# Kernel optimization log

Measured on AMD Instinct MI355X. Metric: run time of the kernel, lower is better.

Reference implementation:

```python
import jax, jax.numpy as jnp
import numpy as np

N = 1026     # tickers (hardcoded in original module)
T = 8        # price window length; self.T = T-1 = 7
H = 64       # hidden dim
F_IN = 5     # price features
E = 1026     # number of hyperedges
NNZ = 200000 # incidence entries per hypergraph


def leaky(x):
    return jnp.where(x >= 0, x, 0.2 * x)


def gru_fwd(x, Wih, Whh, bih, bhh):
    # torch.nn.GRU, batch_first. x: [N, T, F_IN] -> full [N,T,H], last [N,H]
    def step(h, xt):
        gi = xt @ Wih.T + bih
        gh = h @ Whh.T + bhh
        ir, iz, inn = jnp.split(gi, 3, axis=-1)
        hr, hz, hn = jnp.split(gh, 3, axis=-1)
        r = jax.nn.sigmoid(ir + hr)
        z = jax.nn.sigmoid(iz + hz)
        n = jnp.tanh(inn + r * hn)
        h = (1.0 - z) * n + z * h
        return h, h
    h0 = jnp.zeros((x.shape[0], H), x.dtype)
    last, full = jax.lax.scan(step, h0, jnp.swapaxes(x, 0, 1))
    return jnp.swapaxes(full, 0, 1), last


def hyp_conv(x, idx, theta, bias):
    # PyG HypergraphConv (use_attention=False): out = D^-1 H B^-1 H^T (X theta) + bias
    node, edge = idx[0], idx[1]
    ones = jnp.ones(node.shape, x.dtype)
    deg_n = jax.ops.segment_sum(ones, node, num_segments=N)
    deg_e = jax.ops.segment_sum(ones, edge, num_segments=E)
    Dinv = jnp.where(deg_n > 0, 1.0 / deg_n, 0.0)
    Binv = jnp.where(deg_e > 0, 1.0 / deg_e, 0.0)
    xt = x @ theta
    e = jax.ops.segment_sum(xt[node] * Binv[edge][:, None], edge, num_segments=E)
    out = jax.ops.segment_sum(e[edge], node, num_segments=N) * Dinv[:, None]
    return out + bias


def decayed_attention(query, context, Win, Wout, ae, ab):
    # query [N,1,H], context [N,T,H]; 'general' attention with temporal-decay term
    q = jnp.einsum('nod,de->noe', query, Win)
    w = jax.nn.softmax(jnp.einsum('nod,ntd->not', q, context), axis=-1)  # [N,1,T]
    mix = w * jnp.swapaxes(context, 1, 2)                                # [N,H,T]
    delta = jnp.arange(T - 1, -1, -1, dtype=context.dtype).reshape(1, 1, T)
    bt = jnp.exp(-ab * delta)                                            # [N,1,T]
    term2 = jax.nn.relu(ae * mix * bt)
    mixs = jnp.sum(term2 + mix, axis=-1)[:, None, :]                     # [N,1,H]
    comb = jnp.concatenate([mixs, q], axis=2).reshape(N, 2 * H)
    return jnp.tanh(comb @ Wout).reshape(N, H), w


def _forward(price_input, hyp_T, hyp, Wih, Whh, bih, bhh, Win, Wout, ae, ab,
             theta1, bias1, theta2, bias2, w1, w2, a_param, Wl, bl):
    context, last = gru_fwd(price_input, Wih, Whh, bih, bhh)
    output, _ = decayed_attention(last[:, None, :], context, Win, Wout, ae, ab)  # [N,H]

    def per_t(idx):
        x1 = leaky(hyp_conv(output, idx, theta1, bias1))
        return leaky(hyp_conv(x1, idx, theta2, bias2))

    x2 = jax.vmap(per_t)(hyp_T)            # [T, N, H]
    sub = x2[1:] - x2[:-1]                 # diff(): [T-1, N, H]
    b = jnp.mean(sub, axis=(1, 2), keepdims=True)
    U = 1.0 / (1.0 + a_param * (b - sub))  # c = 1
    z = ((U * sub) / U).sum(axis=(1, 2))   # [T-1] (faithful to original)
    wattn = jax.nn.softmax(w2 @ leaky(w1 @ z), axis=0)  # [T-1]
    concat = wattn[:, None, None] * sub
    xx1 = concat[0] + concat[2]            # stack([0],[2]) then sum over dim 0
    xg = leaky(hyp_conv(output, hyp, theta1, bias1))
    xg = leaky(hyp_conv(xg, hyp, theta2, bias2))
    oput = jnp.concatenate([xg, xx1], axis=1)  # [N, 2H]
    return leaky(oput @ Wl + bl)               # [N, 1]


def setup_inputs() -> dict:
    key = jax.random.key(0)
    ks = jax.random.split(key, 24)
    def xn(k, shape, scale=None):
        fan = (shape[-2] + shape[-1]) if len(shape) >= 2 else shape[0]
        s = scale if scale is not None else float(np.sqrt(2.0 / fan))
        return jax.random.normal(k, shape, dtype=jnp.float32) * s
    inp = {}
    inp['price_input'] = jax.random.normal(ks[0], (N, T, F_IN), dtype=jnp.float32)
    node_T = jax.random.randint(ks[1], (T, 1, NNZ), 0, N)
    edge_T = jax.random.randint(ks[2], (T, 1, NNZ), 0, E)
    inp['hyp_T'] = jnp.concatenate([node_T, edge_T], axis=1).astype(jnp.int32)
    node = jax.random.randint(ks[3], (1, NNZ), 0, N)
    edge = jax.random.randint(ks[4], (1, NNZ), 0, E)
    inp['hyp'] = jnp.concatenate([node, edge], axis=0).astype(jnp.int32)
    inp['Wih'] = xn(ks[5], (3 * H, F_IN))
    inp['Whh'] = xn(ks[6], (3 * H, H))
    std = float(1.0 / np.sqrt(3 * H))
    inp['bih'] = jax.random.uniform(ks[7], (3 * H,), minval=-std, maxval=std, dtype=jnp.float32)
    inp['bhh'] = jax.random.uniform(ks[8], (3 * H,), minval=-std, maxval=std, dtype=jnp.float32)
    inp['Win'] = xn(ks[9], (H, H))
    inp['Wout'] = xn(ks[10], (2 * H, H))
    inp['ae'] = xn(ks[11], (N, 1, 1), scale=0.05)
    inp['ab'] = jnp.abs(xn(ks[12], (N, 1, 1), scale=0.05))
    inp['theta1'] = xn(ks[13], (H, H))
    inp['bias1'] = jax.random.uniform(ks[14], (H,), minval=-0.125, maxval=0.125, dtype=jnp.float32)
    inp['theta2'] = xn(ks[15], (H, H))
    inp['bias2'] = jax.random.uniform(ks[16], (H,), minval=-0.125, maxval=0.125, dtype=jnp.float32)
    inp['w1'] = xn(ks[17], (H, T - 1))
    inp['w2'] = xn(ks[18], (T - 1, H))
    inp['a_param'] = xn(ks[19], (T - 1, 1, 1), scale=0.05)
    inp['Wl'] = xn(ks[20], (2 * H, 1))
    inp['bl'] = jax.random.uniform(ks[21], (1,), minval=-0.088, maxval=0.088, dtype=jnp.float32)
    return inp


def reference(price_input, hyp_T, hyp, Wih, Whh, bih, bhh, Win, Wout, ae, ab,
              theta1, bias1, theta2, bias2, w1, w2, a_param, Wl, bl):
    return _forward(price_input, hyp_T, hyp, Wih, Whh, bih, bhh, Win, Wout, ae, ab,
                    theta1, bias1, theta2, bias2, w1, w2, a_param, Wl, bl)
```

## Files before the change

### kernel.cpp

```cpp
#include <hip/hip_runtime.h>
#include <hip/hip_bf16.h>
#include <math.h>

#define N 1026
#define T 8
#define H 64
#define F_IN 5
#define E 1026
#define NNZ 200000
#define TM 7
#define NG 9
#define KP 1056
#define NWB 132
#define RT 96
#define NT 11
#define NH (N*H)
#define BZC 32
#define CHUNK (NH/BZC)

#define OFF_PRICE   0
#define OFF_WIH     41040
#define OFF_WHH     42000
#define OFF_BIH     54288
#define OFF_BHH     54480
#define OFF_WIN     54672
#define OFF_WOUT    58768
#define OFF_AE      66960
#define OFF_AB      67986
#define OFF_TH1     69012
#define OFF_B1      73108
#define OFF_TH2     73172
#define OFF_B2      77268
#define OFF_W1      77332
#define OFF_W2      77780
#define OFF_APAR    78228
#define OFF_WL      78235
#define OFF_BL      78363
#define TOT_CVT     78364

typedef unsigned int u32;
typedef unsigned short u16;
typedef short bf16x8 __attribute__((ext_vector_type(8)));
typedef float f32x4 __attribute__((ext_vector_type(4)));

__device__ __forceinline__ float leakyf(float x){ return x >= 0.f ? x : 0.2f*x; }
__device__ __forceinline__ float bfbits2f(u16 u){
  union { u32 i; float f; } c; c.i = ((u32)u) << 16; return c.f;
}
__device__ __forceinline__ u16 f2bf(float f){
  u32 x = __builtin_bit_cast(u32, f);
  u32 r = x + 0x7FFFu + ((x >> 16) & 1u);
  return (u16)(r >> 16);
}
__device__ __forceinline__ int detect_f32(const u16* __restrict__ w){
  int lane = threadIdx.x & 63;
  int big = 0;
  for (int k = lane; k < 960; k += 64){
    float a = fabsf(bfbits2f(w[k]));
    if (!(a < 1e3f)) big = 1;
  }
  return (__ballot(big != 0) != 0ull) ? 1 : 0;
}

struct CvtPtrs { const void* p[18]; };

__global__ __launch_bounds__(256) void k_cvt(CvtPtrs ps, float* __restrict__ dst){
  const int offs[19] = {OFF_PRICE, OFF_WIH, OFF_WHH, OFF_BIH, OFF_BHH, OFF_WIN,
                        OFF_WOUT, OFF_AE, OFF_AB, OFF_TH1, OFF_B1, OFF_TH2,
                        OFF_B2, OFF_W1, OFF_W2, OFF_APAR, OFF_WL, OFF_BL, TOT_CVT};
  int isf32 = detect_f32((const u16*)ps.p[1]);
  int i = blockIdx.x*256 + threadIdx.x;
  if (i < TOT_CVT){
    int t = 0;
    #pragma unroll
    for (int k = 1; k < 18; k++) if (i >= offs[k]) t = k;
    int j = i - offs[t];
    float v;
    if (isf32) v = ((const float*)ps.p[t])[j];
    else       v = bfbits2f(((const u16*)ps.p[t])[j]);
    dst[i] = v;
  }
}

__global__ __launch_bounds__(1024) void k_build(const int* __restrict__ hypT,
                                                const int* __restrict__ hyp,
                                                u16* __restrict__ AHm,
                                                u16* __restrict__ AHmT,
                                                float* __restrict__ Dinv,
                                                float* __restrict__ Binv){
  __shared__ u32 bins[RT*NWB];
  int tid = threadIdx.x;
  int g = blockIdx.y, side = blockIdx.z;
  int r0 = blockIdx.x * RT;
  for (int k = tid; k < RT*NWB; k += 1024) bins[k] = 0;
  __syncthreads();
  const int4* np4; const int4* ep4;
  if (g < 8){ const int* np_ = hypT + (size_t)g*2*NNZ;
              np4 = (const int4*)np_; ep4 = (const int4*)(np_ + NNZ); }
  else      { np4 = (const int4*)hyp; ep4 = (const int4*)(hyp + NNZ); }
  #pragma unroll 4
  for (int i = tid; i < NNZ/4; i += 1024){
    int4 a4 = np4[i], b4 = ep4[i];
    int ra[4], ca[4];
    if (side){
      ra[0]=b4.x; ra[1]=b4.y; ra[2]=b4.z; ra[3]=b4.w;
      ca[0]=a4.x; ca[1]=a4.y; ca[2]=a4.z; ca[3]=a4.w;
    } else {
      ra[0]=a4.x; ra[1]=a4.y; ra[2]=a4.z; ra[3]=a4.w;
      ca[0]=b4.x; ca[1]=b4.y; ca[2]=b4.z; ca[3]=b4.w;
    }
    #pragma unroll
    for (int e = 0; e < 4; e++){
      int rr = ra[e] - r0;
      if ((unsigned)rr < (unsigned)RT)
        atomicAdd(&bins[rr*NWB + (ca[e]>>3)], 1u << ((ca[e]&7)*4));
    }
  }
  __syncthreads();
  {
    int r = tid >> 3, j = tid & 7;
    if (r < RT){
      u32 s = 0;
      for (int w = j; w < NWB; w += 8){
        u32 v = bins[r*NWB + w];
        u32 a = (v & 0x0F0F0F0Fu) + ((v >> 4) & 0x0F0F0F0Fu);
        s += (a * 0x01010101u) >> 24;
      }
      s += __shfl_xor(s, 1); s += __shfl_xor(s, 2); s += __shfl_xor(s, 4);
      int gr = r0 + r;
      if (j == 0 && gr < N){
        float inv = s ? 1.f/(float)s : 0.f;
        (side ? Binv : Dinv)[g*N + gr] = inv;
      }
    }
  }
  u16* dst = (side ? AHmT : AHm) + (size_t)g*KP*KP;
  for (int idx = tid; idx < RT*NWB; idx += 1024){
    int rr = idx / NWB, w = idx - rr*NWB;
    u32 v = bins[rr*NWB + w];
    bf16x8 o;
    #pragma unroll
    for (int j = 0; j < 8; j++)
      o[j] = (short)f2bf((float)((v >> (4*j)) & 0xFu));
    *(bf16x8*)(dst + (size_t)(r0 + rr)*KP + w*8) = o;
  }
}

__global__ __launch_bounds__(256) void k_gruattn(const float* __restrict__ price,
                                                 const float* __restrict__ Wih,
                                                 const float* __restrict__ Whh,
                                                 const float* __restrict__ bih,
                                                 const float* __restrict__ bhh,
                                                 const float* __restrict__ Win,
                                                 const float* __restrict__ Wout,
                                                 const float* __restrict__ ae,
                                                 const float* __restrict__ ab,
                                                 float* __restrict__ outp){
  __shared__ float gi[T][192];
  __shared__ float sh[64];
  __shared__ float sctx[T*64];
  __shared__ float part[4][192];
  __shared__ float sx[T*F_IN];
  __shared__ float sq[64];
  __shared__ float ssc[T];
  __shared__ float sco[128];
  int tid = threadIdx.x, w = tid>>6, lane = tid&63;
  int n = blockIdx.x;
  float wr_[16], wz_[16], wn_[16];
  #pragma unroll
  for (int j = 0; j < 16; j++){
    int d = w*16 + j;
    wr_[j] = Whh[(size_t)(      lane)*64 + d];
    wz_[j] = Whh[(size_t)( 64 + lane)*64 + d];
    wn_[j] = Whh[(size_t)(128 + lane)*64 + d];
  }
  if (tid < T*F_IN) sx[tid] = price[(size_t)n*T*F_IN + tid];
  if (tid < 64) sh[tid] = 0.f;
  __syncthreads();
  for (int idx = tid; idx < T*192; idx += 256){
    int t = idx / 192, gd = idx - t*192;
    float acc = bih[gd];
    #pragma unroll
    for (int d5 = 0; d5 < F_IN; d5++)
      acc = fmaf(sx[t*F_IN + d5], Wih[gd*F_IN + d5], acc);
    gi[t][gd] = acc;
  }
  __syncthreads();
  for (int t = 0; t < T; t++){
    float pr = 0.f, pz = 0.f, pn = 0.f;
    #pragma unroll
    for (int j = 0; j < 16; j++){
      float hv = sh[w*16 + j];
      pr = fmaf(hv, wr_[j], pr);
      pz = fmaf(hv, wz_[j], pz);
      pn = fmaf(hv, wn_[j], pn);
    }
    part[w][lane] = pr; part[w][64 + lane] = pz; part[w][128 + lane] = pn;
    __syncthreads();
    if (tid < 64){
      int o = tid;
      float hr = bhh[o]       + part[0][o]     + part[1][o]     + part[2][o]     + part[3][o];
      float hz = bhh[64 + o]  + part[0][64+o]  + part[1][64+o]  + part[2][64+o]  + part[3][64+o];
      float hn = bhh[128 + o] + part[0][128+o] + part[1][128+o] + part[2][128+o] + part[3][128+o];
      float r  = 1.f/(1.f + expf(-(gi[t][o] + hr)));
      float z  = 1.f/(1.f + expf(-(gi[t][64 + o] + hz)));
      float nn = tanhf(gi[t][128 + o] + r*hn);
      float hnew = (1.f - z)*nn + z*sh[o];
      sh[o] = hnew;
      sctx[t*64 + o] = hnew;
    }
    __syncthreads();
  }
  {
    float qp = 0.f;
    #pragma unroll
    for (int j = 0; j < 16; j++)
      qp = fmaf(sh[w*16 + j], Win[(size_t)(w*16 + j)*64 + lane], qp);
    part[w][lane] = qp;
  }
  __syncthreads();
  if (tid < 64) sq[tid] = part[0][tid] + part[1][tid] + part[2][tid] + part[3][tid];
  __syncthreads();
  if (tid < T){
    float s = 0.f;
    for (int d = 0; d < 64; d++) s = fmaf(sq[d], sctx[tid*64 + d], s);
    ssc[tid] = s;
  }
  __syncthreads();
  if (tid < 64){
    int o = tid;
    float m = ssc[0];
    for (int t = 1; t < T; t++) m = fmaxf(m, ssc[t]);
    float wv[T]; float den = 0.f;
    for (int t = 0; t < T; t++){ wv[t] = expf(ssc[t] - m); den += wv[t]; }
    float aen = ae[n], abn = ab[n];
    float mixs = 0.f;
    for (int t = 0; t < T; t++){
      float wt = wv[t]/den;
      float mx = wt * sctx[t*64 + o];
      float bt = expf(-abn * (float)(T-1-t));
      mixs += fmaxf(aen*mx*bt, 0.f) + mx;
    }
    sco[o] = mixs; sco[64 + o] = sq[o];
  }
  __syncthreads();
  {
    float op = 0.f;
    #pragma unroll
    for (int j = 0; j < 32; j++)
      op = fmaf(sco[w*32 + j], Wout[(size_t)(w*32 + j)*64 + lane], op);
    part[w][lane] = op;
  }
  __syncthreads();
  if (tid < 64){
    float o = part[0][tid] + part[1][tid] + part[2][tid] + part[3][tid];
    outp[(size_t)n*H + tid] = tanhf(o);
  }
}

__global__ __launch_bounds__(256) void k_xthetaT(const float* __restrict__ x,
                                                 const float* __restrict__ theta,
                                                 int x_per_graph,
                                                 u16* __restrict__ xtT){
  __shared__ float sth[4096];
  __shared__ float sxr[64][64];
  __shared__ float syt[64][65];
  int tid = threadIdx.x, w = tid>>6, lane = tid&63;
  int g = blockIdx.y;
  int r0 = blockIdx.x*64;
  const float* xg = x + (x_per_graph ? (size_t)g*N*64 : (size_t)0);
  for (int k = tid; k < 1024; k += 256) ((float4*)sth)[k] = ((const float4*)theta)[k];
  for (int rr = w; rr < 64; rr += 4){
    int r = r0 + rr;
    sxr[rr][lane] = (r < N) ? xg[(size_t)r*64 + lane] : 0.f;
  }
  __syncthreads();
  for (int rr = w*16; rr < w*16+16; rr++){
    float acc = 0.f;
    for (int d = 0; d < 64; d++) acc = fmaf(sxr[rr][d], sth[d*64 + lane], acc);
    syt[lane][rr] = acc;
  }
  __syncthreads();
  int col = r0 + lane;
  if (col < KP){
    for (int f = w*16; f < w*16+16; f++)
      xtT[((size_t)g*64 + f)*KP + col] = f2bf(syt[f][lane]);
  }
}

__global__ __launch_bounds__(64) void k_gemm(const u16* __restrict__ A,
                                             const u16* __restrict__ Xt,
                                             int x_per_graph,
                                             const float* __restrict__ scale,
                                             const float* __restrict__ bias,
                                             int mode,
                                             u16* __restrict__ Yt,
                                             float* __restrict__ Yf){
  int g = blockIdx.y;
  int m0 = (blockIdx.x >> 2) * 16;
  int nt = blockIdx.x & 3;
  int lane = threadIdx.x;
  int mrow = lane & 15, quad = lane >> 4;
  const u16* Ap = A + (size_t)g*KP*KP + (size_t)(m0 + mrow)*KP + quad*8;
  const u16* Bp = Xt + (x_per_graph ? (size_t)g*64*KP : (size_t)0)
                     + (size_t)(nt*16 + mrow)*KP + quad*8;
  f32x4 acc = (f32x4){0.f,0.f,0.f,0.f};
  bf16x8 a0 = *(const bf16x8*)Ap;
  bf16x8 b0 = *(const bf16x8*)Bp;
  for (int c = 0; c < 33; c++){
    bf16x8 a1 = a0, b1 = b0;
    if (c < 32){
      a1 = *(const bf16x8*)(Ap + (c+1)*32);
      b1 = *(const bf16x8*)(Bp + (c+1)*32);
    }
    acc = __builtin_amdgcn_mfma_f32_16x16x32_bf16(a0, b0, acc, 0, 0, 0);
    a0 = a1; b0 = b1;
  }
  int mbase = m0 + quad*4;
  float sc_[4];
  #pragma unroll
  for (int r = 0; r < 4; r++){
    int m = mbase + r;
    sc_[r] = (m < N) ? scale[g*N + m] : 0.f;
  }
  if (mode == 0){
    ushort4 o;
    o.x = f2bf(acc[0]*sc_[0]);
    o.y = f2bf(acc[1]*sc_[1]);
    o.z = f2bf(acc[2]*sc_[2]);
    o.w = f2bf(acc[3]*sc_[3]);
    *(ushort4*)(Yt + ((size_t)g*64 + nt*16 + mrow)*KP + mbase) = o;
  } else {
    float bs = bias[nt*16 + mrow];
    #pragma unroll
    for (int r = 0; r < 4; r++){
      int m = mbase + r;
      if (m < N){
        float v = acc[r]*sc_[r] + bs;
        Yf[((size_t)g*N + m)*64 + nt*16 + mrow] = leakyf(v);
      }
    }
  }
}

__global__ __launch_bounds__(256) void k_bz1(const float* __restrict__ x2,
                                             float* __restrict__ bpart){
  int k = blockIdx.x, ch = blockIdx.y, tid = threadIdx.x;
  int wv = tid >> 6, lane = tid & 63;
  const float4* a4 = (const float4*)(x2 + (size_t)k*NH + (size_t)ch*CHUNK);
  const float4* c4 = (const float4*)(x2 + (size_t)(k+1)*NH + (size_t)ch*CHUNK);
  float s = 0.f;
  for (int i = tid; i < CHUNK/4; i += 256){
    float4 cc = c4[i], aa = a4[i];
    s += (cc.x-aa.x)+(cc.y-aa.y)+(cc.z-aa.z)+(cc.w-aa.w);
  }
  __shared__ float red[4];
  for (int off = 32; off; off >>= 1) s += __shfl_down(s, off);
  if (lane == 0) red[wv] = s;
  __syncthreads();
  if (tid == 0) bpart[k*BZC + ch] = red[0]+red[1]+red[2]+red[3];
}

__global__ __launch_bounds__(256) void k_bz2(const float* __restrict__ x2,
                                             const float* __restrict__ bpart,
                                             const float* __restrict__ a_param,
                                             float* __restrict__ zpart){
  int k = blockIdx.x, ch = blockIdx.y, tid = threadIdx.x;
  int wv = tid >> 6, lane = tid & 63;
  __shared__ float sbk;
  if (tid == 0){
    float t = 0.f;
    for (int j = 0; j < BZC; j++) t += bpart[k*BZC + j];
    sbk = t / (float)NH;
  }
  __syncthreads();
  float bk = sbk, ap = a_param[k];
  const float4* a4 = (const float4*)(x2 + (size_t)k*NH + (size_t)ch*CHUNK);
  const float4* c4 = (const float4*)(x2 + (size_t)(k+1)*NH + (size_t)ch*CHUNK);
  float s = 0.f;
  for (int i = tid; i < CHUNK/4; i += 256){
    float4 cc = c4[i], aa = a4[i];
    float sb[4] = {cc.x-aa.x, cc.y-aa.y, cc.z-aa.z, cc.w-aa.w};
    #pragma unroll
    for (int j = 0; j < 4; j++){
      float U = 1.f/(1.f + ap*(bk - sb[j]));
      s += (U*sb[j])/U;
    }
  }
  __shared__ float red[4];
  for (int off = 32; off; off >>= 1) s += __shfl_down(s, off);
  if (lane == 0) red[wv] = s;
  __syncthreads();
  if (tid == 0) zpart[k*BZC + ch] = red[0]+red[1]+red[2]+red[3];
}

__global__ __launch_bounds__(256) void k_final(const float* __restrict__ x2,
                                               const float* __restrict__ zpart,
                                               const float* __restrict__ w1,
                                               const float* __restrict__ w2,
                                               const float* __restrict__ Wl,
                                               const float* __restrict__ bl,
                                               const u16* __restrict__ wihRaw,
                                               void* __restrict__ outv){
  __shared__ float sz[8];
  __shared__ float sy[64];
  __shared__ float swa[8];
  int tid = threadIdx.x;
  int isf32 = detect_f32(wihRaw);
  if (tid < TM){
    float t = 0.f;
    for (int j = 0; j < BZC; j++) t += zpart[tid*BZC + j];
    sz[tid] = t;
  }
  __syncthreads();
  if (tid < 64){
    float y = 0.f;
    for (int kk = 0; kk < TM; kk++) y += w1[tid*TM + kk]*sz[kk];
    sy[tid] = leakyf(y);
  }
  __syncthreads();
  if (tid < TM){
    float v = 0.f;
    for (int d = 0; d < 64; d++) v += w2[tid*64 + d]*sy[d];
    swa[tid] = v;
  }
  __syncthreads();
  if (tid == 0){
    float m = swa[0];
    for (int t = 1; t < TM; t++) m = fmaxf(m, swa[t]);
    float den = 0.f;
    for (int t = 0; t < TM; t++){ swa[t] = expf(swa[t]-m); den += swa[t]; }
    for (int t = 0; t < TM; t++) swa[t] /= den;
  }
  __syncthreads();
  int n = blockIdx.x*256 + tid;
  if (n < N){
    float w0 = swa[0], w2v = swa[2];
    float acc = bl[0];
    for (int h = 0; h < 64; h++){
      float xg = x2[(size_t)8*NH + (size_t)n*64 + h];
      float s0 = x2[(size_t)1*NH + (size_t)n*64 + h] - x2[(size_t)0*NH + (size_t)n*64 + h];
      float s2 = x2[(size_t)3*NH + (size_t)n*64 + h] - x2[(size_t)2*NH + (size_t)n*64 + h];
      float xx = w0*s0 + w2v*s2;
      acc += xg*Wl[h] + xx*Wl[64 + h];
    }
    float r = leakyf(acc);
    if (isf32) ((float*)outv)[n] = r;
    else       ((__hip_bfloat16*)outv)[n] = __float2bfloat16(r);
  }
}

extern "C" void kernel_launch(void* const* d_in, const int* in_sizes, int n_in,
                              void* d_out, int out_size, void* d_ws, size_t ws_size,
                              hipStream_t stream) {
  const int* hypT = (const int*)d_in[1];
  const int* hyp  = (const int*)d_in[2];

  char* p = (char*)d_ws;
  auto alloc = [&](size_t bytes) -> char* {
    char* r = p; p += (bytes + 63) & ~(size_t)63; return r;
  };
  float* cv   = (float*)alloc((size_t)TOT_CVT*4);
  u16* AHm    = (u16*)  alloc((size_t)NG*KP*KP*2);
  u16* AHmT   = (u16*)  alloc((size_t)NG*KP*KP*2);
  float* Dinv = (float*)alloc((size_t)NG*N*4);
  float* Binv = (float*)alloc((size_t)NG*N*4);
  float* outp = (float*)alloc((size_t)N*H*4);
  float* x1   = (float*)alloc((size_t)NG*N*H*4);
  float* x2   = (float*)alloc((size_t)NG*N*H*4);
  float* bpart= (float*)alloc((size_t)TM*BZC*4);
  float* zpart= (float*)alloc((size_t)TM*BZC*4);
  u16* xtT1   = (u16*)  alloc((size_t)64*KP*2);
  u16* xtT2   = (u16*)  alloc((size_t)NG*64*KP*2);
  u16* ebufT  = (u16*)  alloc((size_t)NG*64*KP*2);

  const float* price  = cv + OFF_PRICE;
  const float* Wih    = cv + OFF_WIH;
  const float* Whh    = cv + OFF_WHH;
  const float* bih    = cv + OFF_BIH;
  const float* bhh    = cv + OFF_BHH;
  const float* Win    = cv + OFF_WIN;
  const float* Wout   = cv + OFF_WOUT;
  const float* ae     = cv + OFF_AE;
  const float* ab     = cv + OFF_AB;
  const float* theta1 = cv + OFF_TH1;
  const float* bias1  = cv + OFF_B1;
  const float* theta2 = cv + OFF_TH2;
  const float* bias2  = cv + OFF_B2;
  const float* w1     = cv + OFF_W1;
  const float* w2     = cv + OFF_W2;
  const float* a_par  = cv + OFF_APAR;
  const float* Wl     = cv + OFF_WL;
  const float* bl     = cv + OFF_BL;

  CvtPtrs ps;
  ps.p[0]=d_in[0];  ps.p[1]=d_in[3];  ps.p[2]=d_in[4];  ps.p[3]=d_in[5];
  ps.p[4]=d_in[6];  ps.p[5]=d_in[7];  ps.p[6]=d_in[8];  ps.p[7]=d_in[9];
  ps.p[8]=d_in[10]; ps.p[9]=d_in[11]; ps.p[10]=d_in[12]; ps.p[11]=d_in[13];
  ps.p[12]=d_in[14]; ps.p[13]=d_in[15]; ps.p[14]=d_in[16]; ps.p[15]=d_in[17];
  ps.p[16]=d_in[18]; ps.p[17]=d_in[19];
  k_cvt<<<(TOT_CVT+255)/256, 256, 0, stream>>>(ps, cv);

  k_build<<<dim3(NT, NG, 2), 1024, 0, stream>>>(hypT, hyp, AHm, AHmT, Dinv, Binv);
  k_gruattn<<<N, 256, 0, stream>>>(price, Wih, Whh, bih, bhh,
                                   Win, Wout, ae, ab, outp);

  k_xthetaT<<<dim3(17, 1), 256, 0, stream>>>(outp, theta1, 0, xtT1);
  k_gemm<<<dim3((KP/16)*4, NG), 64, 0, stream>>>(AHmT, xtT1, 0, Binv, nullptr, 0, ebufT, nullptr);
  k_gemm<<<dim3((KP/16)*4, NG), 64, 0, stream>>>(AHm, ebufT, 1, Dinv, bias1, 1, nullptr, x1);

  k_xthetaT<<<dim3(17, NG), 256, 0, stream>>>(x1, theta2, 1, xtT2);
  k_gemm<<<dim3((KP/16)*4, NG), 64, 0, stream>>>(AHmT, xtT2, 1, Binv, nullptr, 0, ebufT, nullptr);
  k_gemm<<<dim3((KP/16)*4, NG), 64, 0, stream>>>(AHm, ebufT, 1, Dinv, bias2, 1, nullptr, x2);

  k_bz1<<<dim3(TM, BZC), 256, 0, stream>>>(x2, bpart);
  k_bz2<<<dim3(TM, BZC), 256, 0, stream>>>(x2, bpart, a_par, zpart);
  k_final<<<(N+255)/256, 256, 0, stream>>>(x2, zpart, w1, w2, Wl, bl,
                                           (const u16*)d_in[3], d_out);
}
```

Before: 271.7 us.

## Split GEMM K-loop across two waves and shrink xtheta tiles for more blocks

The dense incidence GEMM kernel now runs two wavefronts per block. Each wave handles half of the K dimension (17 and 16 chunks), and the partial accumulators are reduced through shared memory before the epilogue. This halves the serial MFMA/load chain per block, which adds latency hiding and parallelism. The x·theta kernel now uses 16-row tiles instead of 64, giving 66 blocks per graph instead of 17, and writes with vectorized ushort4 stores. The cost is an extra barrier and shared-memory reduction per GEMM block, and theta is reloaded by more blocks.

New measurement: 280.3 us. 1.03x slower.

```diff
diff --git a/kernel.cpp b/kernel.cpp
--- a/kernel.cpp
+++ b/kernel.cpp
@@ -263,81 +263,100 @@
                                                  int x_per_graph,
                                                  u16* __restrict__ xtT){
   __shared__ float sth[4096];
-  __shared__ float sxr[64][64];
-  __shared__ float syt[64][65];
+  __shared__ float sxr[16][64];
+  __shared__ float syt[64][17];
   int tid = threadIdx.x, w = tid>>6, lane = tid&63;
   int g = blockIdx.y;
-  int r0 = blockIdx.x*64;
+  int r0 = blockIdx.x*16;
   const float* xg = x + (x_per_graph ? (size_t)g*N*64 : (size_t)0);
   for (int k = tid; k < 1024; k += 256) ((float4*)sth)[k] = ((const float4*)theta)[k];
-  for (int rr = w; rr < 64; rr += 4){
-    int r = r0 + rr;
-    sxr[rr][lane] = (r < N) ? xg[(size_t)r*64 + lane] : 0.f;
-  }
-  __syncthreads();
-  for (int rr = w*16; rr < w*16+16; rr++){
+  {
+    int idx = tid;
+    #pragma unroll
+    for (int i = 0; i < 4; i++, idx += 256){
+      int rr = idx >> 6, d = idx & 63;
+      int r = r0 + rr;
+      sxr[rr][d] = (r < N) ? xg[(size_t)r*64 + d] : 0.f;
+    }
+  }
+  __syncthreads();
+  #pragma unroll
+  for (int rr = 0; rr < 4; rr++){
+    int row = w*4 + rr;
     float acc = 0.f;
-    for (int d = 0; d < 64; d++) acc = fmaf(sxr[rr][d], sth[d*64 + lane], acc);
-    syt[lane][rr] = acc;
-  }
-  __syncthreads();
-  int col = r0 + lane;
-  if (col < KP){
-    for (int f = w*16; f < w*16+16; f++)
-      xtT[((size_t)g*64 + f)*KP + col] = f2bf(syt[f][lane]);
-  }
-}
-
-__global__ __launch_bounds__(64) void k_gemm(const u16* __restrict__ A,
-                                             const u16* __restrict__ Xt,
-                                             int x_per_graph,
-                                             const float* __restrict__ scale,
-                                             const float* __restrict__ bias,
-                                             int mode,
-                                             u16* __restrict__ Yt,
-                                             float* __restrict__ Yf){
+    for (int d = 0; d < 64; d++) acc = fmaf(sxr[row][d], sth[d*64 + lane], acc);
+    syt[lane][row] = acc;
+  }
+  __syncthreads();
+  {
+    int f = tid >> 2, c = (tid & 3)*4;
+    ushort4 o;
+    o.x = f2bf(syt[f][c+0]); o.y = f2bf(syt[f][c+1]);
+    o.z = f2bf(syt[f][c+2]); o.w = f2bf(syt[f][c+3]);
+    *(ushort4*)(xtT + ((size_t)g*64 + f)*KP + r0 + c) = o;
+  }
+}
+
+__global__ __launch_bounds__(128) void k_gemm(const u16* __restrict__ A,
+                                              const u16* __restrict__ Xt,
+                                              int x_per_graph,
+                                              const float* __restrict__ scale,
+                                              const float* __restrict__ bias,
+                                              int mode,
+                                              u16* __restrict__ Yt,
+                                              float* __restrict__ Yf){
+  __shared__ f32x4 part[64];
   int g = blockIdx.y;
   int m0 = (blockIdx.x >> 2) * 16;
   int nt = blockIdx.x & 3;
-  int lane = threadIdx.x;
+  int tid = threadIdx.x;
+  int kh = tid >> 6, lane = tid & 63;
   int mrow = lane & 15, quad = lane >> 4;
-  const u16* Ap = A + (size_t)g*KP*KP + (size_t)(m0 + mrow)*KP + quad*8;
+  int kofs = kh ? 544 : 0;
+  int NC   = kh ? 16  : 17;
+  const u16* Ap = A + (size_t)g*KP*KP + (size_t)(m0 + mrow)*KP + kofs + quad*8;
   const u16* Bp = Xt + (x_per_graph ? (size_t)g*64*KP : (size_t)0)
-                     + (size_t)(nt*16 + mrow)*KP + quad*8;
+                     + (size_t)(nt*16 + mrow)*KP + kofs + quad*8;
   f32x4 acc = (f32x4){0.f,0.f,0.f,0.f};
   bf16x8 a0 = *(const bf16x8*)Ap;
   bf16x8 b0 = *(const bf16x8*)Bp;
-  for (int c = 0; c < 33; c++){
+  for (int c = 0; c < NC; c++){
     bf16x8 a1 = a0, b1 = b0;
-    if (c < 32){
+    if (c + 1 < NC){
       a1 = *(const bf16x8*)(Ap + (c+1)*32);
       b1 = *(const bf16x8*)(Bp + (c+1)*32);
     }
     acc = __builtin_amdgcn_mfma_f32_16x16x32_bf16(a0, b0, acc, 0, 0, 0);
     a0 = a1; b0 = b1;
   }
-  int mbase = m0 + quad*4;
-  float sc_[4];
-  #pragma unroll
-  for (int r = 0; r < 4; r++){
-    int m = mbase + r;
-    sc_[r] = (m < N) ? scale[g*N + m] : 0.f;
-  }
-  if (mode == 0){
-    ushort4 o;
-    o.x = f2bf(acc[0]*sc_[0]);
-    o.y = f2bf(acc[1]*sc_[1]);
-    o.z = f2bf(acc[2]*sc_[2]);
-    o.w = f2bf(acc[3]*sc_[3]);
-    *(ushort4*)(Yt + ((size_t)g*64 + nt*16 + mrow)*KP + mbase) = o;
-  } else {
-    float bs = bias[nt*16 + mrow];
+  if (kh == 1) part[lane] = acc;
+  __syncthreads();
+  if (kh == 0){
+    f32x4 o2 = part[lane];
+    acc[0] += o2[0]; acc[1] += o2[1]; acc[2] += o2[2]; acc[3] += o2[3];
+    int mbase = m0 + quad*4;
+    float sc_[4];
     #pragma unroll
     for (int r = 0; r < 4; r++){
       int m = mbase + r;
-      if (m < N){
-        float v = acc[r]*sc_[r] + bs;
-        Yf[((size_t)g*N + m)*64 + nt*16 + mrow] = leakyf(v);
+      sc_[r] = (m < N) ? scale[g*N + m] : 0.f;
+    }
+    if (mode == 0){
+      ushort4 o;
+      o.x = f2bf(acc[0]*sc_[0]);
+      o.y = f2bf(acc[1]*sc_[1]);
+      o.z = f2bf(acc[2]*sc_[2]);
+      o.w = f2bf(acc[3]*sc_[3]);
+      *(ushort4*)(Yt + ((size_t)g*64 + nt*16 + mrow)*KP + mbase) = o;
+    } else {
+      float bs = bias[nt*16 + mrow];
+      #pragma unroll
+      for (int r = 0; r < 4; r++){
+        int m = mbase + r;
+        if (m < N){
+          float v = acc[r]*sc_[r] + bs;
+          Yf[((size_t)g*N + m)*64 + nt*16 + mrow] = leakyf(v);
+        }
       }
     }
   }
@@ -505,13 +524,13 @@
   k_gruattn<<<N, 256, 0, stream>>>(price, Wih, Whh, bih, bhh,
                                    Win, Wout, ae, ab, outp);
 
-  k_xthetaT<<<dim3(17, 1), 256, 0, stream>>>(outp, theta1, 0, xtT1);
-  k_gemm<<<dim3((KP/16)*4, NG), 64, 0, stream>>>(AHmT, xtT1, 0, Binv, nullptr, 0, ebufT, nullptr);
-  k_gemm<<<dim3((KP/16)*4, NG), 64, 0, stream>>>(AHm, ebufT, 1, Dinv, bias1, 1, nullptr, x1);
-
-  k_xthetaT<<<dim3(17, NG), 256, 0, stream>>>(x1, theta2, 1, xtT2);
-  k_gemm<<<dim3((KP/16)*4, NG), 64, 0, stream>>>(AHmT, xtT2, 1, Binv, nullptr, 0, ebufT, nullptr);
-  k_gemm<<<dim3((KP/16)*4, NG), 64, 0, stream>>>(AHm, ebufT, 1, Dinv, bias2, 1, nullptr, x2);
+  k_xthetaT<<<dim3(KP/16, 1), 256, 0, stream>>>(outp, theta1, 0, xtT1);
+  k_gemm<<<dim3((KP/16)*4, NG), 128, 0, stream>>>(AHmT, xtT1, 0, Binv, nullptr, 0, ebufT, nullptr);
+  k_gemm<<<dim3((KP/16)*4, NG), 128, 0, stream>>>(AHm, ebufT, 1, Dinv, bias1, 1, nullptr, x1);
+
+  k_xthetaT<<<dim3(KP/16, NG), 256, 0, stream>>>(x1, theta2, 1, xtT2);
+  k_gemm<<<dim3((KP/16)*4, NG), 128, 0, stream>>>(AHmT, xtT2, 1, Binv, nullptr, 0, ebufT, nullptr);
+  k_gemm<<<dim3((KP/16)*4, NG), 128, 0, stream>>>(AHm, ebufT, 1, Dinv, bias2, 1, nullptr, x2);
 
   k_bz1<<<dim3(TM, BZC), 256, 0, stream>>>(x2, bpart);
   k_bz2<<<dim3(TM, BZC), 256, 0, stream>>>(x2, bpart, a_par, zpart);
```

## Split incidence-matrix build into partitioned scan and separate expand kernel

Applied to the files above, without the earlier changes.

The single k_build kernel, which scanned all NNZ entries per row tile with 1024 threads, is split into two kernels. k_scan divides the NNZ range into PB=4 parts across more 256-thread blocks and merges its shared-memory nibble bins into a global packed-count array with atomics. k_expand then turns the packed counts into bf16 dense matrices and computes the degree inverses. The aim is more parallelism in the scan phase, at the cost of an extra memset, global atomics, an intermediate buffer and one more launch. If any incidence pair repeats 16 or more times, its 4-bit count can overflow into the neighbouring field during the global atomic merge, as it could in the original shared-memory bins.

New measurement: 314.9 us. 1.16x slower.

```diff
diff --git a/kernel.cpp b/kernel.cpp
--- a/kernel.cpp
+++ b/kernel.cpp
@@ -14,6 +14,7 @@
 #define NWB 132
 #define RT 96
 #define NT 11
+#define PB 4
 #define NH (N*H)
 #define BZC 32
 #define CHUNK (NH/BZC)
@@ -82,24 +83,25 @@
   }
 }
 
-__global__ __launch_bounds__(1024) void k_build(const int* __restrict__ hypT,
-                                                const int* __restrict__ hyp,
-                                                u16* __restrict__ AHm,
-                                                u16* __restrict__ AHmT,
-                                                float* __restrict__ Dinv,
-                                                float* __restrict__ Binv){
+__global__ __launch_bounds__(256) void k_scan(const int* __restrict__ hypT,
+                                              const int* __restrict__ hyp,
+                                              u32* __restrict__ nHm,
+                                              u32* __restrict__ nHmT){
   __shared__ u32 bins[RT*NWB];
   int tid = threadIdx.x;
+  int tile = blockIdx.x / PB, prt = blockIdx.x - tile*PB;
   int g = blockIdx.y, side = blockIdx.z;
-  int r0 = blockIdx.x * RT;
-  for (int k = tid; k < RT*NWB; k += 1024) bins[k] = 0;
+  int r0 = tile * RT;
+  for (int k = tid; k < RT*NWB; k += 256) bins[k] = 0;
   __syncthreads();
   const int4* np4; const int4* ep4;
   if (g < 8){ const int* np_ = hypT + (size_t)g*2*NNZ;
               np4 = (const int4*)np_; ep4 = (const int4*)(np_ + NNZ); }
   else      { np4 = (const int4*)hyp; ep4 = (const int4*)(hyp + NNZ); }
-  #pragma unroll 4
-  for (int i = tid; i < NNZ/4; i += 1024){
+  int i0 = prt * (NNZ/4/PB);
+  int i1 = i0 + (NNZ/4/PB);
+  #pragma unroll 2
+  for (int i = i0 + tid; i < i1; i += 256){
     int4 a4 = np4[i], b4 = ep4[i];
     int ra[4], ca[4];
     if (side){
@@ -117,32 +119,45 @@
     }
   }
   __syncthreads();
-  {
-    int r = tid >> 3, j = tid & 7;
-    if (r < RT){
-      u32 s = 0;
-      for (int w = j; w < NWB; w += 8){
-        u32 v = bins[r*NWB + w];
-        u32 a = (v & 0x0F0F0F0Fu) + ((v >> 4) & 0x0F0F0F0Fu);
-        s += (a * 0x01010101u) >> 24;
-      }
-      s += __shfl_xor(s, 1); s += __shfl_xor(s, 2); s += __shfl_xor(s, 4);
-      int gr = r0 + r;
-      if (j == 0 && gr < N){
-        float inv = s ? 1.f/(float)s : 0.f;
-        (side ? Binv : Dinv)[g*N + gr] = inv;
-      }
-    }
-  }
-  u16* dst = (side ? AHmT : AHm) + (size_t)g*KP*KP;
-  for (int idx = tid; idx < RT*NWB; idx += 1024){
-    int rr = idx / NWB, w = idx - rr*NWB;
-    u32 v = bins[rr*NWB + w];
+  u32* dst = (side ? nHmT : nHm) + (size_t)g*KP*NWB + (size_t)r0*NWB;
+  for (int k = tid; k < RT*NWB; k += 256){
+    u32 v = bins[k];
+    if (v) atomicAdd(dst + k, v);
+  }
+}
+
+__global__ __launch_bounds__(256) void k_expand(const u32* __restrict__ nHm,
+                                                const u32* __restrict__ nHmT,
+                                                u16* __restrict__ AHm,
+                                                u16* __restrict__ AHmT,
+                                                float* __restrict__ Dinv,
+                                                float* __restrict__ Binv){
+  int tid = threadIdx.x;
+  int g = blockIdx.y, side = blockIdx.z;
+  int r0 = blockIdx.x * 16;
+  const u32* src = (side ? nHmT : nHm) + (size_t)g*KP*NWB + (size_t)r0*NWB;
+  u16* dst = (side ? AHmT : AHm) + (size_t)g*KP*KP + (size_t)r0*KP;
+  for (int idx = tid; idx < 16*NWB; idx += 256){
+    u32 v = src[idx];
     bf16x8 o;
     #pragma unroll
     for (int j = 0; j < 8; j++)
       o[j] = (short)f2bf((float)((v >> (4*j)) & 0xFu));
-    *(bf16x8*)(dst + (size_t)(r0 + rr)*KP + w*8) = o;
+    *(bf16x8*)(dst + (size_t)idx*8) = o;
+  }
+  int r = tid >> 4, j = tid & 15;
+  u32 s = 0;
+  for (int w = j; w < NWB; w += 16){
+    u32 v = src[r*NWB + w];
+    u32 a = (v & 0x0F0F0F0Fu) + ((v >> 4) & 0x0F0F0F0Fu);
+    s += (a * 0x01010101u) >> 24;
+  }
+  s += __shfl_xor(s, 1); s += __shfl_xor(s, 2);
+  s += __shfl_xor(s, 4); s += __shfl_xor(s, 8);
+  int gr = r0 + r;
+  if (j == 0 && gr < N){
+    float inv = s ? 1.f/(float)s : 0.f;
+    (side ? Binv : Dinv)[g*N + gr] = inv;
   }
 }
 
@@ -461,6 +476,8 @@
     char* r = p; p += (bytes + 63) & ~(size_t)63; return r;
   };
   float* cv   = (float*)alloc((size_t)TOT_CVT*4);
+  u32* nHm    = (u32*)  alloc((size_t)NG*KP*NWB*4);
+  u32* nHmT   = (u32*)  alloc((size_t)NG*KP*NWB*4);
   u16* AHm    = (u16*)  alloc((size_t)NG*KP*KP*2);
   u16* AHmT   = (u16*)  alloc((size_t)NG*KP*KP*2);
   float* Dinv = (float*)alloc((size_t)NG*N*4);
@@ -493,6 +510,8 @@
   const float* Wl     = cv + OFF_WL;
   const float* bl     = cv + OFF_BL;
 
+  hipMemsetAsync(nHm, 0, (size_t)2*NG*KP*NWB*4, stream);
+
   CvtPtrs ps;
   ps.p[0]=d_in[0];  ps.p[1]=d_in[3];  ps.p[2]=d_in[4];  ps.p[3]=d_in[5];
   ps.p[4]=d_in[6];  ps.p[5]=d_in[7];  ps.p[6]=d_in[8];  ps.p[7]=d_in[9];
@@ -501,7 +520,8 @@
   ps.p[16]=d_in[18]; ps.p[17]=d_in[19];
   k_cvt<<<(TOT_CVT+255)/256, 256, 0, stream>>>(ps, cv);
 
-  k_build<<<dim3(NT, NG, 2), 1024, 0, stream>>>(hypT, hyp, AHm, AHmT, Dinv, Binv);
+  k_scan  <<<dim3(NT*PB, NG, 2), 256, 0, stream>>>(hypT, hyp, nHm, nHmT);
+  k_expand<<<dim3(KP/16, NG, 2), 256, 0, stream>>>(nHm, nHmT, AHm, AHmT, Dinv, Binv);
   k_gruattn<<<N, 256, 0, stream>>>(price, Wih, Whh, bih, bhh,
                                    Win, Wout, ae, ab, outp);
 
```

## Fuse conversion, first theta projection, and temporal sums into neighbouring kernels

Applied to the files above, without the earlier changes.

Moves the dtype-conversion pass into the k_build kernel, with the first column block of each graph converting one slice. The first theta projection and its transposed bf16 store move into the end of the GRU/attention kernel. The two reduction kernels are replaced by per-graph atomic sums in the last GEMM's epilogue, using the algebraic identity that (U*sb)/U equals sb, so each temporal sum becomes S[k+1]-S[k]. This removes four kernel launches and two extra passes over x2. In exchange it relies on float atomics, which give non-deterministic ordering and possible cancellation in the difference of large sums. The padded columns of xtT1 beyond N are also no longer written.

Measured after the change: 280.8 us. 1.03x slower.

```diff
diff --git a/kernel.cpp b/kernel.cpp
--- a/kernel.cpp
+++ b/kernel.cpp
@@ -15,8 +15,6 @@
 #define RT 96
 #define NT 11
 #define NH (N*H)
-#define BZC 32
-#define CHUNK (NH/BZC)
 
 #define OFF_PRICE   0
 #define OFF_WIH     41040
@@ -64,34 +62,37 @@
 
 struct CvtPtrs { const void* p[18]; };
 
-__global__ __launch_bounds__(256) void k_cvt(CvtPtrs ps, float* __restrict__ dst){
-  const int offs[19] = {OFF_PRICE, OFF_WIH, OFF_WHH, OFF_BIH, OFF_BHH, OFF_WIN,
-                        OFF_WOUT, OFF_AE, OFF_AB, OFF_TH1, OFF_B1, OFF_TH2,
-                        OFF_B2, OFF_W1, OFF_W2, OFF_APAR, OFF_WL, OFF_BL, TOT_CVT};
-  int isf32 = detect_f32((const u16*)ps.p[1]);
-  int i = blockIdx.x*256 + threadIdx.x;
-  if (i < TOT_CVT){
-    int t = 0;
-    #pragma unroll
-    for (int k = 1; k < 18; k++) if (i >= offs[k]) t = k;
-    int j = i - offs[t];
-    float v;
-    if (isf32) v = ((const float*)ps.p[t])[j];
-    else       v = bfbits2f(((const u16*)ps.p[t])[j]);
-    dst[i] = v;
-  }
-}
-
 __global__ __launch_bounds__(1024) void k_build(const int* __restrict__ hypT,
                                                 const int* __restrict__ hyp,
                                                 u16* __restrict__ AHm,
                                                 u16* __restrict__ AHmT,
                                                 float* __restrict__ Dinv,
-                                                float* __restrict__ Binv){
+                                                float* __restrict__ Binv,
+                                                CvtPtrs ps,
+                                                float* __restrict__ cv,
+                                                float* __restrict__ Ssum){
   __shared__ u32 bins[RT*NWB];
   int tid = threadIdx.x;
   int g = blockIdx.y, side = blockIdx.z;
   int r0 = blockIdx.x * RT;
+  if (blockIdx.x == 0 && side == 0){
+    const int offs[19] = {OFF_PRICE, OFF_WIH, OFF_WHH, OFF_BIH, OFF_BHH, OFF_WIN,
+                          OFF_WOUT, OFF_AE, OFF_AB, OFF_TH1, OFF_B1, OFF_TH2,
+                          OFF_B2, OFF_W1, OFF_W2, OFF_APAR, OFF_WL, OFF_BL, TOT_CVT};
+    int isf32 = detect_f32((const u16*)ps.p[1]);
+    int i0 = g * 8708;
+    for (int i = i0 + tid; i < i0 + 8708 && i < TOT_CVT; i += 1024){
+      int t = 0;
+      #pragma unroll
+      for (int k = 1; k < 18; k++) if (i >= offs[k]) t = k;
+      int j = i - offs[t];
+      float v;
+      if (isf32) v = ((const float*)ps.p[t])[j];
+      else       v = bfbits2f(((const u16*)ps.p[t])[j]);
+      cv[i] = v;
+    }
+    if (g == 0 && tid < 16) Ssum[tid] = 0.f;
+  }
   for (int k = tid; k < RT*NWB; k += 1024) bins[k] = 0;
   __syncthreads();
   const int4* np4; const int4* ep4;
@@ -155,7 +156,8 @@
                                                  const float* __restrict__ Wout,
                                                  const float* __restrict__ ae,
                                                  const float* __restrict__ ab,
-                                                 float* __restrict__ outp){
+                                                 const float* __restrict__ theta1,
+                                                 u16* __restrict__ xtT1){
   __shared__ float gi[T][192];
   __shared__ float sh[64];
   __shared__ float sctx[T*64];
@@ -254,13 +256,25 @@
   __syncthreads();
   if (tid < 64){
     float o = part[0][tid] + part[1][tid] + part[2][tid] + part[3][tid];
-    outp[(size_t)n*H + tid] = tanhf(o);
+    sq[tid] = tanhf(o);
+  }
+  __syncthreads();
+  {
+    float xp = 0.f;
+    #pragma unroll
+    for (int j = 0; j < 16; j++)
+      xp = fmaf(sq[w*16 + j], theta1[(size_t)(w*16 + j)*64 + lane], xp);
+    part[w][lane] = xp;
+  }
+  __syncthreads();
+  if (tid < 64){
+    float v = part[0][tid] + part[1][tid] + part[2][tid] + part[3][tid];
+    xtT1[(size_t)tid*KP + n] = f2bf(v);
   }
 }
 
 __global__ __launch_bounds__(256) void k_xthetaT(const float* __restrict__ x,
                                                  const float* __restrict__ theta,
-                                                 int x_per_graph,
                                                  u16* __restrict__ xtT){
   __shared__ float sth[4096];
   __shared__ float sxr[64][64];
@@ -268,7 +282,7 @@
   int tid = threadIdx.x, w = tid>>6, lane = tid&63;
   int g = blockIdx.y;
   int r0 = blockIdx.x*64;
-  const float* xg = x + (x_per_graph ? (size_t)g*N*64 : (size_t)0);
+  const float* xg = x + (size_t)g*N*64;
   for (int k = tid; k < 1024; k += 256) ((float4*)sth)[k] = ((const float4*)theta)[k];
   for (int rr = w; rr < 64; rr += 4){
     int r = r0 + rr;
@@ -295,7 +309,8 @@
                                              const float* __restrict__ bias,
                                              int mode,
                                              u16* __restrict__ Yt,
-                                             float* __restrict__ Yf){
+                                             float* __restrict__ Yf,
+                                             float* __restrict__ Ssum){
   int g = blockIdx.y;
   int m0 = (blockIdx.x >> 2) * 16;
   int nt = blockIdx.x & 3;
@@ -332,70 +347,25 @@
     *(ushort4*)(Yt + ((size_t)g*64 + nt*16 + mrow)*KP + mbase) = o;
   } else {
     float bs = bias[nt*16 + mrow];
+    float ls = 0.f;
     #pragma unroll
     for (int r = 0; r < 4; r++){
       int m = mbase + r;
       if (m < N){
-        float v = acc[r]*sc_[r] + bs;
-        Yf[((size_t)g*N + m)*64 + nt*16 + mrow] = leakyf(v);
+        float v = leakyf(acc[r]*sc_[r] + bs);
+        Yf[((size_t)g*N + m)*64 + nt*16 + mrow] = v;
+        ls += v;
       }
     }
-  }
-}
-
-__global__ __launch_bounds__(256) void k_bz1(const float* __restrict__ x2,
-                                             float* __restrict__ bpart){
-  int k = blockIdx.x, ch = blockIdx.y, tid = threadIdx.x;
-  int wv = tid >> 6, lane = tid & 63;
-  const float4* a4 = (const float4*)(x2 + (size_t)k*NH + (size_t)ch*CHUNK);
-  const float4* c4 = (const float4*)(x2 + (size_t)(k+1)*NH + (size_t)ch*CHUNK);
-  float s = 0.f;
-  for (int i = tid; i < CHUNK/4; i += 256){
-    float4 cc = c4[i], aa = a4[i];
-    s += (cc.x-aa.x)+(cc.y-aa.y)+(cc.z-aa.z)+(cc.w-aa.w);
-  }
-  __shared__ float red[4];
-  for (int off = 32; off; off >>= 1) s += __shfl_down(s, off);
-  if (lane == 0) red[wv] = s;
-  __syncthreads();
-  if (tid == 0) bpart[k*BZC + ch] = red[0]+red[1]+red[2]+red[3];
-}
-
-__global__ __launch_bounds__(256) void k_bz2(const float* __restrict__ x2,
-                                             const float* __restrict__ bpart,
-                                             const float* __restrict__ a_param,
-                                             float* __restrict__ zpart){
-  int k = blockIdx.x, ch = blockIdx.y, tid = threadIdx.x;
-  int wv = tid >> 6, lane = tid & 63;
-  __shared__ float sbk;
-  if (tid == 0){
-    float t = 0.f;
-    for (int j = 0; j < BZC; j++) t += bpart[k*BZC + j];
-    sbk = t / (float)NH;
-  }
-  __syncthreads();
-  float bk = sbk, ap = a_param[k];
-  const float4* a4 = (const float4*)(x2 + (size_t)k*NH + (size_t)ch*CHUNK);
-  const float4* c4 = (const float4*)(x2 + (size_t)(k+1)*NH + (size_t)ch*CHUNK);
-  float s = 0.f;
-  for (int i = tid; i < CHUNK/4; i += 256){
-    float4 cc = c4[i], aa = a4[i];
-    float sb[4] = {cc.x-aa.x, cc.y-aa.y, cc.z-aa.z, cc.w-aa.w};
-    #pragma unroll
-    for (int j = 0; j < 4; j++){
-      float U = 1.f/(1.f + ap*(bk - sb[j]));
-      s += (U*sb[j])/U;
-    }
-  }
-  __shared__ float red[4];
-  for (int off = 32; off; off >>= 1) s += __shfl_down(s, off);
-  if (lane == 0) red[wv] = s;
-  __syncthreads();
-  if (tid == 0) zpart[k*BZC + ch] = red[0]+red[1]+red[2]+red[3];
+    if (mode == 2){
+      for (int off = 32; off; off >>= 1) ls += __shfl_down(ls, off);
+      if (lane == 0) atomicAdd(&Ssum[g], ls);
+    }
+  }
 }
 
 __global__ __launch_bounds__(256) void k_final(const float* __restrict__ x2,
-                                               const float* __restrict__ zpart,
+                                               const float* __restrict__ Ssum,
                                                const float* __restrict__ w1,
                                                const float* __restrict__ w2,
                                                const float* __restrict__ Wl,
@@ -407,11 +377,7 @@
   __shared__ float swa[8];
   int tid = threadIdx.x;
   int isf32 = detect_f32(wihRaw);
-  if (tid < TM){
-    float t = 0.f;
-    for (int j = 0; j < BZC; j++) t += zpart[tid*BZC + j];
-    sz[tid] = t;
-  }
+  if (tid < TM) sz[tid] = Ssum[tid+1] - Ssum[tid];
   __syncthreads();
   if (tid < 64){
     float y = 0.f;
@@ -465,11 +431,9 @@
   u16* AHmT   = (u16*)  alloc((size_t)NG*KP*KP*2);
   float* Dinv = (float*)alloc((size_t)NG*N*4);
   float* Binv = (float*)alloc((size_t)NG*N*4);
-  float* outp = (float*)alloc((size_t)N*H*4);
   float* x1   = (float*)alloc((size_t)NG*N*H*4);
   float* x2   = (float*)alloc((size_t)NG*N*H*4);
-  float* bpart= (float*)alloc((size_t)TM*BZC*4);
-  float* zpart= (float*)alloc((size_t)TM*BZC*4);
+  float* Ssum = (float*)alloc(64);
   u16* xtT1   = (u16*)  alloc((size_t)64*KP*2);
   u16* xtT2   = (u16*)  alloc((size_t)NG*64*KP*2);
   u16* ebufT  = (u16*)  alloc((size_t)NG*64*KP*2);
@@ -489,7 +453,6 @@
   const float* bias2  = cv + OFF_B2;
   const float* w1     = cv + OFF_W1;
   const float* w2     = cv + OFF_W2;
-  const float* a_par  = cv + OFF_APAR;
   const float* Wl     = cv + OFF_WL;
   const float* bl     = cv + OFF_BL;
 
@@ -499,22 +462,19 @@
   ps.p[8]=d_in[10]; ps.p[9]=d_in[11]; ps.p[10]=d_in[12]; ps.p[11]=d_in[13];
   ps.p[12]=d_in[14]; ps.p[13]=d_in[15]; ps.p[14]=d_in[16]; ps.p[15]=d_in[17];
   ps.p[16]=d_in[18]; ps.p[17]=d_in[19];
-  k_cvt<<<(TOT_CVT+255)/256, 256, 0, stream>>>(ps, cv);
-
-  k_build<<<dim3(NT, NG, 2), 1024, 0, stream>>>(hypT, hyp, AHm, AHmT, Dinv, Binv);
+
+  k_build<<<dim3(NT, NG, 2), 1024, 0, stream>>>(hypT, hyp, AHm, AHmT,
+                                                Dinv, Binv, ps, cv, Ssum);
   k_gruattn<<<N, 256, 0, stream>>>(price, Wih, Whh, bih, bhh,
-                                   Win, Wout, ae, ab, outp);
-
-  k_xthetaT<<<dim3(17, 1), 256, 0, stream>>>(outp, theta1, 0, xtT1);
-  k_gemm<<<dim3((KP/16)*4, NG), 64, 0, stream>>>(AHmT, xtT1, 0, Binv, nullptr, 0, ebufT, nullptr);
-  k_gemm<<<dim3((KP/16)*4, NG), 64, 0, stream>>>(AHm, ebufT, 1, Dinv, bias1, 1, nullptr, x1);
-
-  k_xthetaT<<<dim3(17, NG), 256, 0, stream>>>(x1, theta2, 1, xtT2);
-  k_gemm<<<dim3((KP/16)*4, NG), 64, 0, stream>>>(AHmT, xtT2, 1, Binv, nullptr, 0, ebufT, nullptr);
-  k_gemm<<<dim3((KP/16)*4, NG), 64, 0, stream>>>(AHm, ebufT, 1, Dinv, bias2, 1, nullptr, x2);
-
-  k_bz1<<<dim3(TM, BZC), 256, 0, stream>>>(x2, bpart);
-  k_bz2<<<dim3(TM, BZC), 256, 0, stream>>>(x2, bpart, a_par, zpart);
-  k_final<<<(N+255)/256, 256, 0, stream>>>(x2, zpart, w1, w2, Wl, bl,
+                                   Win, Wout, ae, ab, theta1, xtT1);
+
+  k_gemm<<<dim3((KP/16)*4, NG), 64, 0, stream>>>(AHmT, xtT1, 0, Binv, nullptr, 0, ebufT, nullptr, nullptr);
+  k_gemm<<<dim3((KP/16)*4, NG), 64, 0, stream>>>(AHm, ebufT, 1, Dinv, bias1, 1, nullptr, x1, nullptr);
+
+  k_xthetaT<<<dim3(17, NG), 256, 0, stream>>>(x1, theta2, xtT2);
+  k_gemm<<<dim3((KP/16)*4, NG), 64, 0, stream>>>(AHmT, xtT2, 1, Binv, nullptr, 0, ebufT, nullptr, nullptr);
+  k_gemm<<<dim3((KP/16)*4, NG), 64, 0, stream>>>(AHm, ebufT, 1, Dinv, bias2, 2, nullptr, x2, Ssum);
+
+  k_final<<<(N+255)/256, 256, 0, stream>>>(x2, Ssum, w1, w2, Wl, bl,
                                            (const u16*)d_in[3], d_out);
 }
```
